# Kernel optimization log

Hardware: AMD Instinct MI355X
Metric: run time of the kernel (lower is better)

Reference implementation:

```python
import jax, jax.numpy as jnp
import numpy as np

DIM = 256
HEADS = 8
G = 8            # group (window) size per axis
POS_DIM = 16     # (dim // 4) // 4
MLP_HIDDEN = 4 * DIM


def layernorm(x, g, b, eps=1e-5):
    m = x.mean(-1, keepdims=True)
    v = ((x - m) ** 2).mean(-1, keepdims=True)
    return (x - m) / jnp.sqrt(v + eps) * g + b


def setup_inputs() -> dict:
    key = jax.random.key(0)
    ks = jax.random.split(key, 32)
    s = 0.02
    d = {}
    d['x'] = jax.random.normal(ks[0], (1, 32768, DIM), jnp.float32)
    d['y'] = jax.random.normal(ks[1], (1, 32768, DIM), jnp.float32)
    d['n1_g'] = jnp.ones((DIM,), jnp.float32)
    d['n1_b'] = jnp.zeros((DIM,), jnp.float32)
    d['qkv_w'] = jax.random.normal(ks[2], (DIM, 3 * DIM), jnp.float32) * s
    d['qkv_b'] = jnp.zeros((3 * DIM,), jnp.float32)
    d['pp_w'] = jax.random.normal(ks[3], (3, POS_DIM), jnp.float32) * s
    d['pp_b'] = jnp.zeros((POS_DIM,), jnp.float32)
    d['p1_lng'] = jnp.ones((POS_DIM,), jnp.float32)
    d['p1_lnb'] = jnp.zeros((POS_DIM,), jnp.float32)
    d['p1_w'] = jax.random.normal(ks[4], (POS_DIM, POS_DIM), jnp.float32) * s
    d['p1_b'] = jnp.zeros((POS_DIM,), jnp.float32)
    d['p2_lng'] = jnp.ones((POS_DIM,), jnp.float32)
    d['p2_lnb'] = jnp.zeros((POS_DIM,), jnp.float32)
    d['p2_w'] = jax.random.normal(ks[5], (POS_DIM, POS_DIM), jnp.float32) * s
    d['p2_b'] = jnp.zeros((POS_DIM,), jnp.float32)
    d['p3_lng'] = jnp.ones((POS_DIM,), jnp.float32)
    d['p3_lnb'] = jnp.zeros((POS_DIM,), jnp.float32)
    d['p3_w'] = jax.random.normal(ks[6], (POS_DIM, HEADS), jnp.float32) * s
    d['p3_b'] = jnp.zeros((HEADS,), jnp.float32)
    d['proj_w'] = jax.random.normal(ks[7], (DIM, DIM), jnp.float32) * s
    d['proj_b'] = jnp.zeros((DIM,), jnp.float32)
    d['n2_g'] = jnp.ones((DIM,), jnp.float32)
    d['n2_b'] = jnp.zeros((DIM,), jnp.float32)
    d['fc1_w'] = jax.random.normal(ks[8], (DIM, MLP_HIDDEN), jnp.float32) * s
    d['fc1_b'] = jnp.zeros((MLP_HIDDEN,), jnp.float32)
    d['fc2_w'] = jax.random.normal(ks[9], (MLP_HIDDEN, DIM), jnp.float32) * s
    d['fc2_b'] = jnp.zeros((DIM,), jnp.float32)
    d['H'] = 32
    d['W'] = 32
    d['D'] = 32
    return d


def reference(x, y, n1_g, n1_b, qkv_w, qkv_b, pp_w, pp_b,
              p1_lng, p1_lnb, p1_w, p1_b, p2_lng, p2_lnb, p2_w, p2_b,
              p3_lng, p3_lnb, p3_w, p3_b, proj_w, proj_b,
              n2_g, n2_b, fc1_w, fc1_b, fc2_w, fc2_b, H, W, D):
    B, L, C = x.shape
    nh, g = HEADS, G
    hd = C // nh
    shortcut = x
    xn = layernorm(x, n1_g, n1_b)
    xv = xn.reshape(B, H, W, D, C)
    yv = y.reshape(B, H, W, D, C)  # note: y is NOT normed in the original

    # SDA window partition (H,W,D divisible by g -> no padding, zero mask)
    def part(t):
        t = t.reshape(B, H // g, g, W // g, g, D // g, g, C)
        t = t.transpose(0, 1, 3, 5, 2, 4, 6, 7)
        return t.reshape(-1, g * g * g, C)

    xg, yg = part(xv), part(yv)
    B_, N, _ = xg.shape

    # original quirk: self.qkv used for BOTH x and y (qkv_y layer unused)
    qkv = (xg @ qkv_w + qkv_b).reshape(B_, N, 3, nh, hd).transpose(2, 0, 3, 1, 4)
    qkv_y = (yg @ qkv_w + qkv_b).reshape(B_, N, 3, nh, hd).transpose(2, 0, 3, 1, 4)
    q = qkv[0] * (hd ** -0.5)
    k_y, v_y = qkv_y[1], qkv_y[2]

    attn = jnp.einsum('bhnd,bhmd->bhnm', q, k_y)  # [B_, nh, N, N]

    # dynamic relative position bias (small MLP + gather)
    rng = jnp.arange(1 - g, g)
    bh, bw, bd = jnp.meshgrid(rng, rng, rng, indexing='ij')
    biases = jnp.stack([bh, bw, bd], -1).reshape(-1, 3).astype(x.dtype)  # [(2g-1)^3, 3]
    pos = biases @ pp_w + pp_b
    pos = jax.nn.relu(layernorm(pos, p1_lng, p1_lnb)) @ p1_w + p1_b
    pos = jax.nn.relu(layernorm(pos, p2_lng, p2_lnb)) @ p2_w + p2_b
    pos = jax.nn.relu(layernorm(pos, p3_lng, p3_lnb)) @ p3_w + p3_b  # [(2g-1)^3, nh]

    c = jnp.arange(g)
    ch, cw, cd = jnp.meshgrid(c, c, c, indexing='ij')
    cf = jnp.stack([ch, cw, cd], 0).reshape(3, -1)          # [3, g^3]
    rel = (cf[:, :, None] - cf[:, None, :]).transpose(1, 2, 0) + (g - 1)
    idx = rel[..., 0] * (2 * g - 1) * (2 * g - 1) + rel[..., 1] * (2 * g - 1) + rel[..., 2]
    bias = pos[idx].transpose(2, 0, 1)  # [nh, N, N]

    attn = jax.nn.softmax(attn + bias[None], axis=-1)
    out = jnp.einsum('bhnm,bhmd->bhnd', attn, v_y).transpose(0, 2, 1, 3).reshape(B_, N, C)
    out = out @ proj_w + proj_b

    # reverse window partition
    out = out.reshape(B, H // g, W // g, D // g, g, g, g, C)
    out = out.transpose(0, 1, 4, 2, 5, 3, 6, 7).reshape(B, H * W * D, C)

    x = shortcut + out
    x2 = layernorm(x, n2_g, n2_b)
    h = jax.nn.gelu(x2 @ fc1_w + fc1_b, approximate=False)
    x = x + (h @ fc2_w + fc2_b)
    return x
```

## Files before the change

### kernel.cpp

```cpp
#include <hip/hip_runtime.h>
#include <cstdint>
#include <cstddef>

typedef unsigned int u32;
typedef unsigned short u16;
typedef __attribute__((ext_vector_type(8))) short bf16x8;
typedef __attribute__((ext_vector_type(4))) float f32x4;

#define DEV __device__ __forceinline__

DEV u16 f2b(float f){ u32 x = __float_as_uint(f); x += 0x7fffu + ((x>>16)&1u); return (u16)(x>>16); }
DEV u32 pk2(float a, float b){
  u32 r;
  asm("v_cvt_pk_bf16_f32 %0, %1, %2" : "=v"(r) : "v"(a), "v"(b));
  return r;
}

DEV void gll16(const void* g, void* l){
  __builtin_amdgcn_global_load_lds((const __attribute__((address_space(1))) u32*)g,
                                   (__attribute__((address_space(3))) u32*)l, 16, 0, 0);
}

DEV void win_n(int r, int& win, int& n){
  int d_ = r & 31, w_ = (r>>5)&31, h_ = r>>10;
  win = ((h_>>3)<<4) | ((w_>>3)<<2) | (d_>>3);
  n   = ((h_&7)<<6)  | ((w_&7)<<3)  | (d_&7);
}
DEV int tok_of(int r){
  int win = r>>9, nn = r&511;
  int bh = win>>4, bw=(win>>2)&3, bd=win&3;
  int ih = nn>>6,  iw=(nn>>3)&7,  id=nn&7;
  return ((bh*8+ih)<<10) | ((bw*8+iw)<<5) | (bd*8+id);
}


__global__ void wtrall_k(const float* __restrict__ qkv_w, const float* __restrict__ proj_w,
                         const float* __restrict__ fc1_w, const float* __restrict__ fc2_w,
                         u16* __restrict__ qkvT, u16* __restrict__ projT,
                         u16* __restrict__ fc1T, u16* __restrict__ fc2T){
  int f = blockIdx.x*256 + threadIdx.x;
  const float* w; u16* wt; int g; bool k10 = false; int N;
  if (f < 196608)      { w=qkv_w;  wt=qkvT;  g=f;        N=768;  }
  else if (f < 262144) { w=proj_w; wt=projT; g=f-196608; N=256;  }
  else if (f < 524288) { w=fc1_w;  wt=fc1T;  g=f-262144; N=1024; }
  else                 { w=fc2_w;  wt=fc2T;  g=f-524288; N=256;  k10=true; }
  int n = k10 ? (g>>10) : (g>>8);
  int k = k10 ? (g&1023) : (g&255);
  wt[g] = f2b(w[(size_t)k*N + n]);
}

template<int NOUT>
DEV void pstage(float* v, const float* g, const float* b, const float* W, const float* bb){
  float m = 0.f;
  #pragma unroll
  for (int i=0;i<16;i++) m += v[i];
  m *= 0.0625f;
  float q = 0.f;
  #pragma unroll
  for (int i=0;i<16;i++){ float d=v[i]-m; q += d*d; }
  float rs = rsqrtf(q*0.0625f + 1e-5f);
  float u[16];
  #pragma unroll
  for (int i=0;i<16;i++){ float t = (v[i]-m)*rs*g[i] + b[i]; u[i] = t>0.f?t:0.f; }
  #pragma unroll
  for (int o=0;o<NOUT;o++){
    float s = bb[o];
    #pragma unroll
    for (int kk=0;kk<16;kk++) s += u[kk]*W[kk*NOUT+o];
    v[o] = s;
  }
}

__global__ void posmlp_k(const float* pp_w, const float* pp_b,
                         const float* g1, const float* b1, const float* w1, const float* bb1,
                         const float* g2, const float* b2, const float* w2, const float* bb2,
                         const float* g3, const float* b3, const float* w3, const float* bb3,
                         float* __restrict__ posb){
  int i = blockIdx.x*256 + threadIdx.x;
  if (i >= 3375) return;
  int t = i;
  int bd = t % 15; t /= 15;
  int bw = t % 15; t /= 15;
  int bh = t;
  float fh = (float)(bh-7), fw = (float)(bw-7), fd = (float)(bd-7);
  float v[16];
  #pragma unroll
  for (int o=0;o<16;o++) v[o] = fh*pp_w[o] + fw*pp_w[16+o] + fd*pp_w[32+o] + pp_b[o];
  pstage<16>(v, g1,b1,w1,bb1);
  pstage<16>(v, g2,b2,w2,bb2);
  pstage<8> (v, g3,b3,w3,bb3);
  #pragma unroll
  for (int h=0;h<8;h++) posb[(size_t)h*3376 + i] = v[h] * 1.4426950408889634f;
}

struct GemmP {
  const u16* A;
  const float* Af32;
  const float* lng; const float* lnb;
  const u16* Bt;
  int K;
  const float* bvec;
  float scale;
  const float* add32;
  float* out32;
  u16* out16;
  u16* out16b;
};

template<int MODE>
DEV void epi(const GemmP& p, int r, int c, float val){
  if constexpr (MODE==0){
    float qv = (val + p.bvec[c]) * p.scale;
    int win, n; win_n(r, win, n);
    int hh = c>>5, dd = c&31;
    p.out16[((size_t)((win*8+hh)*512 + n)<<5) + dd] = f2b(qv);
  } else if constexpr (MODE==1){
    float ov = val + p.bvec[c];
    int win, n; win_n(r, win, n);
    int cc = c & 255;
    int hh = cc>>5, dd = cc&31;
    size_t base = (size_t)(win*8+hh)*16384;
    if (c < 256){
      int nc = n>>4, ln2 = ((dd>>3)<<4)|(n&15), jj = dd&7;
      p.out16[base + (size_t)(nc*64+ln2)*8 + jj] = f2b(ov);
    } else {
      int fi = ((n>>5)<<1) | (dd>>4);
      int ln2 = (((n>>3)&3)<<4)|(dd&15), jj = n&7;
      p.out16b[base + (size_t)(fi*64+ln2)*8 + jj] = f2b(ov);
    }
  } else if constexpr (MODE==2){
    int l = tok_of(r);
    size_t o = (size_t)l*256 + c;
    p.out32[o] = val + p.bvec[c] + p.add32[o];
  } else if constexpr (MODE==3){
    float u = val + p.bvec[c];
    float e = exp2f(u*(2.3022083f + 0.1029437f*u*u));
    float ge = u*e*__builtin_amdgcn_rcpf(e+1.f);
    p.out16[(size_t)r*1024 + c] = f2b(ge);
  } else {
    size_t o = (size_t)r*256 + c;
    p.out32[o] = val + p.bvec[c] + p.add32[o];
  }
}

template<int MODE, int STG, int NT>
__global__ __launch_bounds__(512, 2)
void gemmA_k(GemmP p){
  __shared__ u16 smem[16384];
  const int tid = threadIdx.x;
  const int wid = tid>>6, lane = tid&63;
  const int lr = lane&15, lg = lane>>4;
  const int m0 = blockIdx.x*64;
  const int wm = (wid>>2)*32, wn = (wid&3)*32;
  const int T = NT*8;
  const f32x4 z4 = {0.f,0.f,0.f,0.f};

  if constexpr (STG==3){
    #pragma unroll
    for (int it=0; it<4; ++it){
      int f = it*8 + wid;
      int rt = f>>3, kt = f&7;
      int row = m0 + rt*16 + lr;
      gll16(p.A + ((size_t)((row>>9)*8 + kt)*512 + (row&511))*32 + lg*8,
            (char*)smem + f*1024 + lane*16);
    }
    asm volatile("s_waitcnt vmcnt(0)" ::: "memory");
    __builtin_amdgcn_s_barrier();
  } else {
    const int row = wid*8 + (lane>>3);
    const int sub = lane&7;
    const float* src = p.Af32 + (size_t)(m0+row)*256;
    float xv[32];
    #pragma unroll
    for (int j=0;j<8;j++){
      float4 v = *(const float4*)(src + j*32 + sub*4);
      xv[j*4+0]=v.x; xv[j*4+1]=v.y; xv[j*4+2]=v.z; xv[j*4+3]=v.w;
    }
    float mu=0.f, rs=1.f;
    if constexpr (STG==1){
      float s=0.f;
      #pragma unroll
      for (int i2=0;i2<32;i2++) s += xv[i2];
      s += __shfl_xor(s,1); s += __shfl_xor(s,2); s += __shfl_xor(s,4);
      mu = s*(1.f/256.f);
      float q2=0.f;
      #pragma unroll
      for (int i2=0;i2<32;i2++){ float d=xv[i2]-mu; q2 += d*d; }
      q2 += __shfl_xor(q2,1); q2 += __shfl_xor(q2,2); q2 += __shfl_xor(q2,4);
      rs = rsqrtf(q2*(1.f/256.f) + 1e-5f);
    }
    const int rt = wid>>1, q = (wid&1)*8 + (lane>>3);
    #pragma unroll
    for (int j=0;j<8;j++){
      float o0,o1,o2,o3;
      if constexpr (STG==1){
        float4 gg = *(const float4*)(p.lng + j*32 + sub*4);
        float4 bb = *(const float4*)(p.lnb + j*32 + sub*4);
        o0=(xv[j*4+0]-mu)*rs*gg.x+bb.x; o1=(xv[j*4+1]-mu)*rs*gg.y+bb.y;
        o2=(xv[j*4+2]-mu)*rs*gg.z+bb.z; o3=(xv[j*4+3]-mu)*rs*gg.w+bb.w;
      } else {
        o0=xv[j*4+0]; o1=xv[j*4+1]; o2=xv[j*4+2]; o3=xv[j*4+3];
      }
      int f = rt*8 + j;
      *(uint2*)((char*)smem + f*1024 + (sub>>1)*256 + q*16 + (sub&1)*8)
          = make_uint2((u32)f2b(o0) | ((u32)f2b(o1)<<16),
                       (u32)f2b(o2) | ((u32)f2b(o3)<<16));
    }
    asm volatile("s_waitcnt lgkmcnt(0)" ::: "memory");
    __builtin_amdgcn_s_barrier();
  }
  bf16x8 areg[2][8];
  #pragma unroll
  for (int i=0;i<2;i++)
    #pragma unroll
    for (int kt=0;kt<8;kt++){
      int f = ((wid>>2)*2 + i)*8 + kt;
      areg[i][kt] = *(const bf16x8*)((const char*)smem + f*1024 + lane*16);
    }
  asm volatile("s_waitcnt lgkmcnt(0)" ::: "memory");
  __builtin_amdgcn_s_barrier();

  u16* lB = smem;
  auto stageB = [&](int buf, int t){
    int j = t>>3, kt = t&7;
    gll16(p.Bt + (size_t)(j*128 + wid*16 + lr)*256 + kt*32 + lg*8,
          (char*)lB + buf*8192 + wid*1024 + lane*16);
  };
  stageB(0, 0);
  if (T > 1) stageB(1, 1);

  constexpr int EPIW = (MODE==2) ? 33 : 17;
  f32x4 acc[2][2];
  #pragma unroll
  for (int i=0;i<2;i++){ acc[i][0]=z4; acc[i][1]=z4; }

  int cur = 0, stg = 2, t = 0;
  for (int j=0; j<NT; ++j){
    #pragma unroll
    for (int kt=0; kt<8; ++kt, ++t){
      if (t+1 >= T)        asm volatile("s_waitcnt vmcnt(0)" ::: "memory");
      else if (kt==0 && t) asm volatile("s_waitcnt vmcnt(%0)" :: "i"(EPIW) : "memory");
      else                 asm volatile("s_waitcnt vmcnt(1)" ::: "memory");
      __builtin_amdgcn_s_barrier();
      __builtin_amdgcn_sched_barrier(0);
      bf16x8 bfr[2];
      #pragma unroll
      for (int jj=0;jj<2;jj++)
        bfr[jj] = *(const bf16x8*)((const char*)lB + cur*8192 + ((wid&3)*2+jj)*1024 + lane*16);
      #pragma unroll
      for (int i=0;i<2;i++)
        #pragma unroll
        for (int jj=0;jj<2;jj++)
          acc[i][jj] = __builtin_amdgcn_mfma_f32_16x16x32_bf16(areg[i][kt], bfr[jj], acc[i][jj], 0,0,0);
      __builtin_amdgcn_sched_barrier(0);
      if (kt == 7){
        int n0 = j*128;
        #pragma unroll
        for (int i=0;i<2;i++)
          #pragma unroll
          for (int jj=0;jj<2;jj++){
            #pragma unroll
            for (int v=0;v<4;v++)
              epi<MODE>(p, m0 + wm + i*16 + lg*4 + v, n0 + wn + jj*16 + lr, acc[i][jj][v]);
            acc[i][jj] = z4;
          }
      }
      if (t+2 < T) stageB(stg, t+2);
      cur = (cur==2)?0:cur+1;
      stg = (stg==2)?0:stg+1;
    }
  }
}

__global__ __launch_bounds__(512, 2)
void gemmW_k(GemmP p){
  __shared__ u16 lA[3][2048];
  __shared__ u16 lB[3][8192];
  const int tid = threadIdx.x;
  const int wid = tid>>6, lane = tid&63;
  const int lr = lane&15, lg = lane>>4;
  const int m0 = blockIdx.x*64;
  const int wm = (wid>>2)*32, wn = (wid&3)*64;
  const f32x4 z4 = {0.f,0.f,0.f,0.f};

  auto stage = [&](int buf, int kt){
    {
      int f = wid>>1, half = wid&1;
      if (lane < 32){
        int lg2 = half*2 + (lane>>4);
        gll16(p.A + (size_t)(m0 + f*16 + (lane&15))*1024 + kt*32 + lg2*8,
              (char*)lA[buf] + f*1024 + half*512 + lane*16);
      }
    }
    #pragma unroll
    for (int r=0;r<2;r++){
      int fb = wid*2 + r;
      gll16(p.Bt + (size_t)(fb*16 + lr)*1024 + kt*32 + lg*8,
            (char*)lB[buf] + fb*1024 + lane*16);
    }
  };
  stage(0, 0);
  stage(1, 1);

  f32x4 acc[2][4];
  #pragma unroll
  for (int i=0;i<2;i++)
    #pragma unroll
    for (int j=0;j<4;j++) acc[i][j] = z4;

  int cur = 0, stg = 2;
  for (int kt=0; kt<32; ++kt){
    if (kt+1 < 32) asm volatile("s_waitcnt vmcnt(3)" ::: "memory");
    else           asm volatile("s_waitcnt vmcnt(0)" ::: "memory");
    __builtin_amdgcn_s_barrier();
    __builtin_amdgcn_sched_barrier(0);
    bf16x8 af[2], bfr[4];
    #pragma unroll
    for (int i=0;i<2;i++){
      int fA = (wid>>2)*2 + i;
      af[i] = *(const bf16x8*)((const char*)lA[cur] + fA*1024 + lane*16);
    }
    #pragma unroll
    for (int j=0;j<4;j++){
      int fB = (wid&3)*4 + j;
      bfr[j] = *(const bf16x8*)((const char*)lB[cur] + fB*1024 + lane*16);
    }
    #pragma unroll
    for (int i=0;i<2;i++)
      #pragma unroll
      for (int j=0;j<4;j++)
        acc[i][j] = __builtin_amdgcn_mfma_f32_16x16x32_bf16(af[i], bfr[j], acc[i][j], 0,0,0);
    __builtin_amdgcn_sched_barrier(0);
    if (kt+2 < 32) stage(stg, kt+2);
    cur = (cur==2)?0:cur+1;
    stg = (stg==2)?0:stg+1;
  }

  #pragma unroll
  for (int i=0;i<2;i++)
    #pragma unroll
    for (int j=0;j<4;j++)
      #pragma unroll
      for (int v=0;v<4;v++)
        epi<4>(p, m0 + wm + i*16 + lg*4 + v, wn + j*16 + lr, acc[i][j][v]);
}

__global__ __launch_bounds__(512, 2)
void attn_k(const u16* __restrict__ Q, const u16* __restrict__ Kf,
            const u16* __restrict__ Vf, const float* __restrict__ posb,
            u16* __restrict__ outF){
  __shared__ u16 lK[16384];
  __shared__ u16 lV[16384];
  __shared__ float lPf[3392];
  const int bid = blockIdx.x;
  const int hh = bid&7;
  const int tid = threadIdx.x, wid = tid>>6, lane = tid&63;
  const int lr = lane&15, lg = lane>>4;
  const u16* Kb = Kf + (size_t)bid*16384;
  const u16* Vb = Vf + (size_t)bid*16384;
  const u16* Qb = Q  + (size_t)bid*16384;
  #pragma unroll
  for (int r=0;r<4;r++){
    int off = (r*512 + tid)*16;
    gll16((const char*)Kb + off, (char*)lK + off);
    gll16((const char*)Vb + off, (char*)lV + off);
  }
  const float* ptab = posb + (size_t)hh*3376;
  for (int t=tid; t<3375; t+=512) lPf[t] = ptab[t];
  __syncthreads();
  const f32x4 z4 = {0.f,0.f,0.f,0.f};
  const bf16x8 ones = {(short)0x3F80,(short)0x3F80,(short)0x3F80,(short)0x3F80,
                       (short)0x3F80,(short)0x3F80,(short)0x3F80,(short)0x3F80};

  for (int ch=0; ch<4; ++ch){
    const int r0 = wid*64 + ch*16;
    const int q  = r0 + lr;
    const int Ab = (q>>6)*225 + ((q>>3)&7)*15 + (q&7) + 1687 - (lg>>1)*15 - (lg&1)*4;
    bf16x8 qf = *(const bf16x8*)(Qb + (size_t)q*32 + lg*8);
    f32x4 o0 = z4, o1 = z4, as_ = z4;
    #pragma unroll
    for (int ph=0; ph<2; ++ph){
      f32x4 sf[16];
      __builtin_amdgcn_s_setprio(1);
      #pragma unroll
      for (int i=0;i<16;i++){
        int nc = ph*16 + i;
        const float* bp = lPf + (Ab - (nc>>2)*225 - (nc&3)*30 - 3);
        f32x4 c; c[0]=bp[3]; c[1]=bp[2]; c[2]=bp[1]; c[3]=bp[0];
        bf16x8 kf = *(const bf16x8*)&lK[(nc*64 + lane)*8];
        sf[i] = __builtin_amdgcn_mfma_f32_16x16x32_bf16(kf, qf, c, 0,0,0);
      }
      __builtin_amdgcn_s_setprio(0);
      #pragma unroll
      for (int i=0;i<16;i++){
        sf[i][0] = exp2f(sf[i][0]);
        sf[i][1] = exp2f(sf[i][1]);
        sf[i][2] = exp2f(sf[i][2]);
        sf[i][3] = exp2f(sf[i][3]);
      }
      #pragma unroll
      for (int kc=0;kc<8;kc++){
        u32 a0 = pk2(sf[2*kc  ][0], sf[2*kc  ][1]);
        u32 a1 = pk2(sf[2*kc  ][2], sf[2*kc  ][3]);
        u32 b0 = pk2(sf[2*kc+1][0], sf[2*kc+1][1]);
        u32 b1 = pk2(sf[2*kc+1][2], sf[2*kc+1][3]);
        asm("v_permlane32_swap_b32 %0, %1" : "+v"(a0), "+v"(b0));
        asm("v_permlane16_swap_b32 %0, %1" : "+v"(a0), "+v"(b0));
        asm("v_permlane32_swap_b32 %0, %1" : "+v"(a1), "+v"(b1));
        asm("v_permlane16_swap_b32 %0, %1" : "+v"(a1), "+v"(b1));
        bf16x8 pf;
        ((u32*)&pf)[0]=a0; ((u32*)&pf)[1]=a1; ((u32*)&pf)[2]=b0; ((u32*)&pf)[3]=b1;
        int kcg = ph*8 + kc;
        bf16x8 v0 = *(const bf16x8*)&lV[(size_t)((kcg*2+0)*64 + lane)*8];
        bf16x8 v1 = *(const bf16x8*)&lV[(size_t)((kcg*2+1)*64 + lane)*8];
        __builtin_amdgcn_s_setprio(1);
        o0  = __builtin_amdgcn_mfma_f32_16x16x32_bf16(pf, v0, o0, 0,0,0);
        o1  = __builtin_amdgcn_mfma_f32_16x16x32_bf16(pf, v1, o1, 0,0,0);
        as_ = __builtin_amdgcn_mfma_f32_16x16x32_bf16(pf, ones, as_, 0,0,0);
        __builtin_amdgcn_s_setprio(0);
      }
    }
    #pragma unroll
    for (int v=0;v<4;v++){
      float inv = 1.0f / as_[v];
      int n = r0 + lg*4 + v;
      size_t base = ((size_t)bid*512 + n)*32;
      outF[base + lr]      = f2b(o0[v]*inv);
      outF[base + 16 + lr] = f2b(o1[v]*inv);
    }
  }
}

extern "C" void kernel_launch(void* const* d_in, const int* in_sizes, int n_in,
                              void* d_out, int out_size, void* d_ws, size_t ws_size,
                              hipStream_t stream){
  const float* x      = (const float*)d_in[0];
  const float* y      = (const float*)d_in[1];
  const float* n1_g   = (const float*)d_in[2];
  const float* n1_b   = (const float*)d_in[3];
  const float* qkv_w  = (const float*)d_in[4];
  const float* qkv_b  = (const float*)d_in[5];
  const float* pp_w   = (const float*)d_in[6];
  const float* pp_b   = (const float*)d_in[7];
  const float* p1_lng = (const float*)d_in[8];
  const float* p1_lnb = (const float*)d_in[9];
  const float* p1_w   = (const float*)d_in[10];
  const float* p1_b   = (const float*)d_in[11];
  const float* p2_lng = (const float*)d_in[12];
  const float* p2_lnb = (const float*)d_in[13];
  const float* p2_w   = (const float*)d_in[14];
  const float* p2_b   = (const float*)d_in[15];
  const float* p3_lng = (const float*)d_in[16];
  const float* p3_lnb = (const float*)d_in[17];
  const float* p3_w   = (const float*)d_in[18];
  const float* p3_b   = (const float*)d_in[19];
  const float* proj_w = (const float*)d_in[20];
  const float* proj_b = (const float*)d_in[21];
  const float* n2_g   = (const float*)d_in[22];
  const float* n2_b   = (const float*)d_in[23];
  const float* fc1_w  = (const float*)d_in[24];
  const float* fc1_b  = (const float*)d_in[25];
  const float* fc2_w  = (const float*)d_in[26];
  const float* fc2_b  = (const float*)d_in[27];
  float* out = (float*)d_out;
  char* ws = (char*)d_ws;

  u16*   qkvT  = (u16*)  (ws + 0);
  u16*   projT = (u16*)  (ws + 393216);
  u16*   fc1T  = (u16*)  (ws + 524288);
  u16*   fc2T  = (u16*)  (ws + 1048576);
  float* posb  = (float*)(ws + 1572864);
  u16*   hbuf  = (u16*)  (ws + 5898240);
  u16*   Qb    = (u16*)  (ws + 39452672);
  u16*   Kfb   = (u16*)  (ws + 56229888);
  u16*   Vfb   = (u16*)  (ws + 73007104);
  u16*   attnF = (u16*)  (ws + 89784320);
  float* xres  = (float*)(ws + 106561536);

  wtrall_k<<<3072,256,0,stream>>>(qkv_w, proj_w, fc1_w, fc2_w, qkvT, projT, fc1T, fc2T);
  posmlp_k<<<14,256,0,stream>>>(pp_w, pp_b,
                                p1_lng,p1_lnb,p1_w,p1_b,
                                p2_lng,p2_lnb,p2_w,p2_b,
                                p3_lng,p3_lnb,p3_w,p3_b, posb);

  GemmP pq; pq.A=nullptr; pq.Af32=x; pq.lng=n1_g; pq.lnb=n1_b;
  pq.Bt=qkvT; pq.K=256; pq.bvec=qkv_b;
  pq.scale=0.17677669529663687f*1.4426950408889634f;
  pq.add32=nullptr; pq.out32=nullptr; pq.out16=Qb; pq.out16b=nullptr;
  gemmA_k<0,1,2><<<512,512,0,stream>>>(pq);

  GemmP pkv; pkv.A=nullptr; pkv.Af32=y; pkv.lng=nullptr; pkv.lnb=nullptr;
  pkv.Bt=qkvT + 256*256; pkv.K=256; pkv.bvec=qkv_b + 256;
  pkv.scale=1.f; pkv.add32=nullptr; pkv.out32=nullptr; pkv.out16=Kfb; pkv.out16b=Vfb;
  gemmA_k<1,2,4><<<512,512,0,stream>>>(pkv);

  attn_k<<<512,512,0,stream>>>(Qb, Kfb, Vfb, posb, attnF);

  GemmP pp; pp.A=attnF; pp.Af32=nullptr; pp.lng=nullptr; pp.lnb=nullptr;
  pp.Bt=projT; pp.K=256; pp.bvec=proj_b;
  pp.scale=1.f; pp.add32=x; pp.out32=xres; pp.out16=nullptr; pp.out16b=nullptr;
  gemmA_k<2,3,2><<<512,512,0,stream>>>(pp);

  GemmP pf1; pf1.A=nullptr; pf1.Af32=xres; pf1.lng=n2_g; pf1.lnb=n2_b;
  pf1.Bt=fc1T; pf1.K=256; pf1.bvec=fc1_b;
  pf1.scale=1.f; pf1.add32=nullptr; pf1.out32=nullptr; pf1.out16=hbuf; pf1.out16b=nullptr;
  gemmA_k<3,1,8><<<512,512,0,stream>>>(pf1);

  GemmP pf2; pf2.A=hbuf; pf2.Af32=nullptr; pf2.lng=nullptr; pf2.lnb=nullptr;
  pf2.Bt=fc2T; pf2.K=1024; pf2.bvec=fc2_b;
  pf2.scale=1.f; pf2.add32=xres; pf2.out32=out; pf2.out16=nullptr; pf2.out16b=nullptr;
  gemmW_k<<<512,512,0,stream>>>(pf2);
}
```

Measured before the change: 252.2 us.

## Write MODE1 K/V epilogue as packed bf16 fragments; read K directly from global

In the QKV GEMM, the K/V half of the output (n0>=256) is now packed to bf16 in registers, permuted with permlane swaps, and stored as 16-byte fragments straight into the attention-ready layout instead of going through per-element epi calls. The waitcnt at the last tile is tuned to match. In the attention kernel, K is no longer staged in LDS: fragments are loaded from global memory inside the QK loop. The positional bias is added after the MFMA, just before exp2, rather than being used as the accumulator init. This cuts LDS use and scattered stores, at the cost of global-load latency on the score MFMAs.

```diff
diff --git a/kernel.cpp b/kernel.cpp
--- a/kernel.cpp
+++ b/kernel.cpp
@@ -229,7 +229,6 @@
   stageB(0, 0);
   if (T > 1) stageB(1, 1);
 
-  constexpr int EPIW = (MODE==2) ? 33 : 17;
   f32x4 acc[2][2];
   #pragma unroll
   for (int i=0;i<2;i++){ acc[i][0]=z4; acc[i][1]=z4; }
@@ -238,9 +237,17 @@
   for (int j=0; j<NT; ++j){
     #pragma unroll
     for (int kt=0; kt<8; ++kt, ++t){
-      if (t+1 >= T)        asm volatile("s_waitcnt vmcnt(0)" ::: "memory");
-      else if (kt==0 && t) asm volatile("s_waitcnt vmcnt(%0)" :: "i"(EPIW) : "memory");
-      else                 asm volatile("s_waitcnt vmcnt(1)" ::: "memory");
+      if (t+1 >= T){
+        asm volatile("s_waitcnt vmcnt(0)" ::: "memory");
+      } else if (kt==0 && t){
+        if constexpr (MODE==2)       asm volatile("s_waitcnt vmcnt(33)" ::: "memory");
+        else if (MODE==1 && NT==4){
+          if (j==3) asm volatile("s_waitcnt vmcnt(3)"  ::: "memory");
+          else      asm volatile("s_waitcnt vmcnt(17)" ::: "memory");
+        } else                       asm volatile("s_waitcnt vmcnt(17)" ::: "memory");
+      } else {
+        asm volatile("s_waitcnt vmcnt(1)" ::: "memory");
+      }
       __builtin_amdgcn_s_barrier();
       __builtin_amdgcn_sched_barrier(0);
       bf16x8 bfr[2];
@@ -255,15 +262,41 @@
       __builtin_amdgcn_sched_barrier(0);
       if (kt == 7){
         int n0 = j*128;
-        #pragma unroll
-        for (int i=0;i<2;i++)
+        if (MODE==1 && n0 >= 256){
           #pragma unroll
-          for (int jj=0;jj<2;jj++){
+          for (int i=0;i<2;i++){
+            float bb0 = p.bvec[n0+wn+lr], bb1 = p.bvec[n0+wn+16+lr];
+            u32 a0 = pk2(acc[i][0][0]+bb0, acc[i][0][1]+bb0);
+            u32 a1 = pk2(acc[i][0][2]+bb0, acc[i][0][3]+bb0);
+            u32 b0 = pk2(acc[i][1][0]+bb1, acc[i][1][1]+bb1);
+            u32 b1 = pk2(acc[i][1][2]+bb1, acc[i][1][3]+bb1);
+            asm("v_permlane32_swap_b32 %0, %1" : "+v"(a0), "+v"(b0));
+            asm("v_permlane16_swap_b32 %0, %1" : "+v"(a0), "+v"(b0));
+            asm("v_permlane32_swap_b32 %0, %1" : "+v"(a1), "+v"(b1));
+            asm("v_permlane16_swap_b32 %0, %1" : "+v"(a1), "+v"(b1));
+            bf16x8 fr;
+            ((u32*)&fr)[0]=a0; ((u32*)&fr)[1]=a1; ((u32*)&fr)[2]=b0; ((u32*)&fr)[3]=b1;
+            int r8 = m0 + wm + i*16 + ((lane>>4)&1)*8;
+            int c  = n0 + wn + ((lane>>5)&1)*16 + lr;
+            int win, n; win_n(r8, win, n);
+            int cc = c & 255, hhh = cc>>5, dd = cc&31;
+            size_t base = (size_t)(win*8+hhh)*16384;
+            int fi  = ((n>>5)<<1) | (dd>>4);
+            int ln2 = (((n>>3)&3)<<4) | (dd&15);
+            *(bf16x8*)(p.out16b + base + (size_t)(fi*64+ln2)*8) = fr;
+            acc[i][0] = z4; acc[i][1] = z4;
+          }
+        } else {
+          #pragma unroll
+          for (int i=0;i<2;i++)
             #pragma unroll
-            for (int v=0;v<4;v++)
-              epi<MODE>(p, m0 + wm + i*16 + lg*4 + v, n0 + wn + jj*16 + lr, acc[i][jj][v]);
-            acc[i][jj] = z4;
-          }
+            for (int jj=0;jj<2;jj++){
+              #pragma unroll
+              for (int v=0;v<4;v++)
+                epi<MODE>(p, m0 + wm + i*16 + lg*4 + v, n0 + wn + jj*16 + lr, acc[i][jj][v]);
+              acc[i][jj] = z4;
+            }
+        }
       }
       if (t+2 < T) stageB(stg, t+2);
       cur = (cur==2)?0:cur+1;
@@ -349,7 +382,6 @@
 void attn_k(const u16* __restrict__ Q, const u16* __restrict__ Kf,
             const u16* __restrict__ Vf, const float* __restrict__ posb,
             u16* __restrict__ outF){
-  __shared__ u16 lK[16384];
   __shared__ u16 lV[16384];
   __shared__ float lPf[3392];
   const int bid = blockIdx.x;
@@ -362,7 +394,6 @@
   #pragma unroll
   for (int r=0;r<4;r++){
     int off = (r*512 + tid)*16;
-    gll16((const char*)Kb + off, (char*)lK + off);
     gll16((const char*)Vb + off, (char*)lV + off);
   }
   const float* ptab = posb + (size_t)hh*3376;
@@ -385,18 +416,18 @@
       #pragma unroll
       for (int i=0;i<16;i++){
         int nc = ph*16 + i;
+        bf16x8 kf = *(const bf16x8*)(Kb + (size_t)(nc*64 + lane)*8);
+        sf[i] = __builtin_amdgcn_mfma_f32_16x16x32_bf16(kf, qf, z4, 0,0,0);
+      }
+      __builtin_amdgcn_s_setprio(0);
+      #pragma unroll
+      for (int i=0;i<16;i++){
+        int nc = ph*16 + i;
         const float* bp = lPf + (Ab - (nc>>2)*225 - (nc&3)*30 - 3);
-        f32x4 c; c[0]=bp[3]; c[1]=bp[2]; c[2]=bp[1]; c[3]=bp[0];
-        bf16x8 kf = *(const bf16x8*)&lK[(nc*64 + lane)*8];
-        sf[i] = __builtin_amdgcn_mfma_f32_16x16x32_bf16(kf, qf, c, 0,0,0);
-      }
-      __builtin_amdgcn_s_setprio(0);
-      #pragma unroll
-      for (int i=0;i<16;i++){
-        sf[i][0] = exp2f(sf[i][0]);
-        sf[i][1] = exp2f(sf[i][1]);
-        sf[i][2] = exp2f(sf[i][2]);
-        sf[i][3] = exp2f(sf[i][3]);
+        sf[i][3] = exp2f(sf[i][3] + bp[0]);
+        sf[i][2] = exp2f(sf[i][2] + bp[1]);
+        sf[i][1] = exp2f(sf[i][1] + bp[2]);
+        sf[i][0] = exp2f(sf[i][0] + bp[3]);
       }
       #pragma unroll
       for (int kc=0;kc<8;kc++){
```

New measurement: 248.5 us. No clear change (-1.4%).
